# Optimization experiments

Measured on AMD Instinct MI355X. Metric: run time of the kernel, lower is better.

The kernel has to match this reference:

```python
import jax, jax.numpy as jnp
import numpy as np

N = 20000      # nodes
E = 640000     # edges (avg degree 32)
IN = 32        # input_dim
HID = 256      # hidden_dim
H = 8          # num_heads
Dh = HID // H  # head_dim = 32
TD = 32        # time_dim
L = 3          # num_layers
OUT = 2


def setup_inputs() -> dict:
    key = jax.random.key(0)
    ks = jax.random.split(key, 20)
    def w(k, sh):
        return (jax.random.normal(k, sh, jnp.float32) * 0.05)
    return {
        "x": jax.random.normal(ks[0], (N, IN), jnp.float32),
        "timestamps": jax.random.uniform(ks[1], (N,), jnp.float32),
        "edge_index": jax.random.randint(ks[2], (2, E), 0, N, jnp.int32),
        "batch": jnp.zeros((N,), jnp.int32),
        "time_freq": jax.random.normal(ks[3], (TD // 2,), jnp.float32),
        "inW": w(ks[4], (IN, HID)), "inb": jnp.zeros((HID,), jnp.float32),
        "qW": w(ks[5], (L, HID + TD, HID)), "qb": jnp.zeros((L, HID), jnp.float32),
        "kW": w(ks[6], (L, HID + TD, HID)), "kb": jnp.zeros((L, HID), jnp.float32),
        "vW": w(ks[7], (L, HID, HID)), "vb": jnp.zeros((L, HID), jnp.float32),
        "oW": w(ks[8], (L, HID, HID)), "ob": jnp.zeros((L, HID), jnp.float32),
        "c1W": w(ks[9], (HID, HID // 2)), "c1b": jnp.zeros((HID // 2,), jnp.float32),
        "c2W": w(ks[10], (HID // 2, OUT)), "c2b": jnp.zeros((OUT,), jnp.float32),
    }


def reference(x, timestamps, time_freq, inW, inb, qW, qb, kW, kb, vW, vb,
              oW, ob, c1W, c1b, c2W, c2b, edge_index, batch):
    n = x.shape[0]
    src, dst = edge_index[0], edge_index[1]

    # Functional time encoding (node-level timestamps branch)
    t = (timestamps - timestamps.min()) / (timestamps.max() - timestamps.min() + 1e-8)
    wt = t[:, None] * time_freq[None, :]                      # [N, TD/2]
    tf = jnp.concatenate([jnp.cos(wt), jnp.sin(wt)], axis=-1)  # [N, TD]

    h = x @ inW + inb                                          # [N, HID]
    scale = 1.0 / np.sqrt(Dh).astype(np.float32)

    for l in range(L):
        xt = jnp.concatenate([h, tf], axis=-1)                 # [N, HID+TD]
        Q = (xt @ qW[l] + qb[l]).reshape(n, H, Dh)
        K = (xt @ kW[l] + kb[l]).reshape(n, H, Dh)
        V = (h @ vW[l] + vb[l]).reshape(n, H, Dh)

        # per-edge attention scores [E, H]
        scores = jnp.einsum('ehd,ehd->eh', Q[dst], K[src]) * scale

        # segment softmax over incoming edges of each dst node
        m = jax.ops.segment_max(scores, dst, num_segments=n)   # [N, H]
        e = jnp.exp(scores - m[dst])
        s = jax.ops.segment_sum(e, dst, num_segments=n)        # [N, H]
        att = e / s[dst]                                       # [E, H]

        msgs = att[..., None] * V[src]                         # [E, H, Dh]
        out = jax.ops.segment_sum(msgs, dst, num_segments=n)   # [N, H, Dh]
        out = out.reshape(n, HID) @ oW[l] + ob[l]
        h = jax.nn.elu(out)

    # global mean pool (single graph: batch all zeros)
    cnt = jax.ops.segment_sum(jnp.ones((n, 1), h.dtype), batch, num_segments=1)
    g = jax.ops.segment_sum(h, batch, num_segments=1) / jnp.maximum(cnt, 1.0)

    logits = jax.nn.relu(g @ c1W + c1b) @ c2W + c2b            # [1, OUT]
    return logits
```

## Files before the change

### kernel.cpp

```cpp
#include <hip/hip_runtime.h>
#include <math.h>

#define HID 256
#define TD 32
#define NL 3
#define C1DIM 128
#define OUTDIM 2
#define QKVW 768

using half8  = __attribute__((ext_vector_type(8))) _Float16;
using half2v = __attribute__((ext_vector_type(2))) _Float16;
using f32x4  = __attribute__((ext_vector_type(4))) float;

typedef __attribute__((address_space(1))) void gbl_void_t;
typedef __attribute__((address_space(3))) void lds_void_t;

__device__ __forceinline__ void load16_to_lds(const void* g, void* l) {
  __builtin_amdgcn_global_load_lds((const gbl_void_t*)g, (lds_void_t*)l, 16, 0, 0);
}

__device__ __forceinline__ float dot8h(half8 a, half8 b, float acc) {
#if __has_builtin(__builtin_amdgcn_fdot2)
  union { half8 v; half2v h2[4]; } ua, ub;
  ua.v = a; ub.v = b;
#pragma unroll
  for (int j = 0; j < 4; ++j) acc = __builtin_amdgcn_fdot2(ua.h2[j], ub.h2[j], acc, false);
  return acc;
#else
#pragma unroll
  for (int j = 0; j < 8; ++j) acc += (float)a[j] * (float)b[j];
  return acc;
#endif
}

__global__ __launch_bounds__(1024) void k_tsmm(const float* __restrict__ ts,
                                               float* __restrict__ mmf,
                                               int* __restrict__ deg, int n) {
  int t = threadIdx.x;
  float lmin = INFINITY, lmax = -INFINITY;
  for (int i = t; i < n; i += 1024) {
    float v = ts[i];
    lmin = fminf(lmin, v);
    lmax = fmaxf(lmax, v);
    deg[i] = 0;
  }
#pragma unroll
  for (int off = 32; off >= 1; off >>= 1) {
    lmin = fminf(lmin, __shfl_xor(lmin, off));
    lmax = fmaxf(lmax, __shfl_xor(lmax, off));
  }
  __shared__ float wmin[16], wmax[16];
  int lane = t & 63, w = t >> 6;
  if (lane == 0) { wmin[w] = lmin; wmax[w] = lmax; }
  __syncthreads();
  if (t == 0) {
    float a = INFINITY, b = -INFINITY;
    for (int i = 0; i < 16; ++i) { a = fminf(a, wmin[i]); b = fmaxf(b, wmax[i]); }
    mmf[0] = a; mmf[1] = b;
  }
}

__global__ void k_enc(const float* __restrict__ ts, const float* __restrict__ freq,
                      const float* __restrict__ mmf, const float* __restrict__ x,
                      _Float16* __restrict__ tfh, _Float16* __restrict__ xh, int n) {
  int idx = blockIdx.x * blockDim.x + threadIdx.x;
  int nt = n * TD;
  if (idx < nt) {
    int node = idx >> 5, j = idx & 31;
    float t = (ts[node] - mmf[0]) / (mmf[1] - mmf[0] + 1e-8f);
    float w = t * freq[j & 15];
    tfh[idx] = (_Float16)((j < 16) ? cosf(w) : sinf(w));
  } else if (idx < nt + n * 32) {
    int i2 = idx - nt;
    xh[i2] = (_Float16)x[i2];
  }
}

#define NB_QKV (NL * 9 * 12)
#define NB_O   (NL * 8 * 4)
#define NB_B   9

__global__ __launch_bounds__(256) void k_prep2(
    const float* __restrict__ qW, const float* __restrict__ kW,
    const float* __restrict__ vW, const float* __restrict__ oW,
    const float* __restrict__ qb, const float* __restrict__ kb,
    const float* __restrict__ vb,
    _Float16* __restrict__ qkvWt, float* __restrict__ qkvb,
    _Float16* __restrict__ oWt) {
  __shared__ _Float16 lds[32][65];
  int bid = blockIdx.x;
  int t = threadIdx.x;
  const int KQ = HID + TD;

  if (bid < NB_QKV) {
    int l = bid / 108;
    int rem = bid - l * 108;
    int kt = rem / 12, ntile = rem - kt * 12;
    int k0 = kt * 32, n0 = ntile * 64;
#pragma unroll
    for (int it = 0; it < 8; ++it) {
      int i = it * 256 + t;
      int kk = i >> 6, nn = i & 63;
      int k = k0 + kk, nrow = n0 + nn;
      float v;
      if (nrow < 256)      v = qW[(size_t)l * KQ * HID + (size_t)k * HID + nrow];
      else if (nrow < 512) v = kW[(size_t)l * KQ * HID + (size_t)k * HID + (nrow - 256)];
      else                 v = (k < HID) ? vW[(size_t)l * HID * HID + (size_t)k * HID + (nrow - 512)] : 0.f;
      lds[kk][nn] = (_Float16)v;
    }
    __syncthreads();
    {
      int nn = t >> 2, kq = (t & 3) * 8;
      _Float16* dst = qkvWt + (size_t)l * QKVW * KQ + (size_t)(n0 + nn) * KQ + k0 + kq;
      half8 v;
#pragma unroll
      for (int j = 0; j < 8; ++j) v[j] = lds[kq + j][nn];
      *(half8*)dst = v;
    }
    return;
  }
  bid -= NB_QKV;

  if (bid < NB_O) {
    int l = bid / 32;
    int rem = bid - l * 32;
    int kt = rem / 4, ntile = rem - kt * 4;
    int k0 = kt * 32, n0 = ntile * 64;
#pragma unroll
    for (int it = 0; it < 8; ++it) {
      int i = it * 256 + t;
      int kk = i >> 6, nn = i & 63;
      lds[kk][nn] = (_Float16)oW[(size_t)l * HID * HID + (size_t)(k0 + kk) * HID + n0 + nn];
    }
    __syncthreads();
    {
      int nn = t >> 2, kq = (t & 3) * 8;
      _Float16* dst = oWt + (size_t)l * HID * HID + (size_t)(n0 + nn) * HID + k0 + kq;
      half8 v;
#pragma unroll
      for (int j = 0; j < 8; ++j) v[j] = lds[kq + j][nn];
      *(half8*)dst = v;
    }
    return;
  }
  bid -= NB_O;

  {
    int idx = bid * 256 + t;
    if (idx < NL * QKVW) {
      int l = idx / QKVW;
      int j = idx - l * QKVW;
      float v;
      if (j < 256)      v = qb[l * HID + j];
      else if (j < 512) v = kb[l * HID + (j - 256)];
      else              v = vb[l * HID + (j - 512)];
      qkvb[idx] = v;
    }
  }
}

__global__ __launch_bounds__(256) void k_fold(const float* __restrict__ inW,
                                              const float* __restrict__ inb,
                                              const float* __restrict__ qW,
                                              const float* __restrict__ kW,
                                              const float* __restrict__ vW,
                                              const float* __restrict__ qb,
                                              const float* __restrict__ kb,
                                              const float* __restrict__ vb,
                                              _Float16* __restrict__ WcT,
                                              float* __restrict__ bc) {
  int idx = blockIdx.x * 256 + threadIdx.x;
  if (idx >= 65 * QKVW) return;
  int j = idx / QKVW;
  int nrow = idx - j * QKVW;
  auto W0 = [&](int c, int nr) -> float {
    if (nr < 256)      return qW[(size_t)c * HID + nr];
    else if (nr < 512) return kW[(size_t)c * HID + (nr - 256)];
    else               return vW[(size_t)c * HID + (nr - 512)];
  };
  if (j < 32) {
    float acc = 0.f;
    for (int c = 0; c < 256; ++c) acc += inW[j * HID + c] * W0(c, nrow);
    WcT[(size_t)nrow * 64 + j] = (_Float16)acc;
  } else if (j < 64) {
    int r = 256 + (j - 32);
    float v = 0.f;
    if (nrow < 256)      v = qW[(size_t)r * HID + nrow];
    else if (nrow < 512) v = kW[(size_t)r * HID + (nrow - 256)];
    WcT[(size_t)nrow * 64 + j] = (_Float16)v;
  } else {
    float acc;
    if (nrow < 256)      acc = qb[nrow];
    else if (nrow < 512) acc = kb[nrow - 256];
    else                 acc = vb[nrow - 512];
    for (int c = 0; c < 256; ++c) acc += inb[c] * W0(c, nrow);
    bc[nrow] = acc;
  }
}

__global__ void k_count(const int* __restrict__ dst, int* deg, int e) {
  int i = blockIdx.x * blockDim.x + threadIdx.x;
  if (i < e) atomicAdd(&deg[dst[i]], 1);
}

__global__ __launch_bounds__(256) void k_scan_part(const int* __restrict__ deg,
                                                   int* __restrict__ bsum, int n) {
  int t = threadIdx.x;
  int idx = blockIdx.x * 256 + t;
  int v = (idx < n) ? deg[idx] : 0;
  int lane = t & 63, w = t >> 6;
  int x = v;
#pragma unroll
  for (int off = 1; off < 64; off <<= 1) {
    int y = __shfl_up(x, off);
    if (lane >= off) x += y;
  }
  __shared__ int ws[4];
  if (lane == 63) ws[w] = x;
  __syncthreads();
  if (t == 0) bsum[blockIdx.x] = ws[0] + ws[1] + ws[2] + ws[3];
}

__global__ __launch_bounds__(64) void k_scan_mid(const int* __restrict__ bsum,
                                                 int* __restrict__ boff, int nb) {
  int lane = threadIdx.x;
  int carry = 0;
  for (int base = 0; base < nb; base += 64) {
    int i = base + lane;
    int v = (i < nb) ? bsum[i] : 0;
    int x = v;
#pragma unroll
    for (int off = 1; off < 64; off <<= 1) {
      int y = __shfl_up(x, off);
      if (lane >= off) x += y;
    }
    if (i < nb) boff[i] = carry + x - v;
    carry += __shfl(x, 63);
  }
}

__global__ __launch_bounds__(256) void k_scan_apply(const int* __restrict__ deg,
                                                    const int* __restrict__ boff,
                                                    int* __restrict__ row_ptr,
                                                    int* __restrict__ cursor, int n, int e) {
  int t = threadIdx.x;
  int idx = blockIdx.x * 256 + t;
  int v = (idx < n) ? deg[idx] : 0;
  int lane = t & 63, w = t >> 6;
  int x = v;
#pragma unroll
  for (int off = 1; off < 64; off <<= 1) {
    int y = __shfl_up(x, off);
    if (lane >= off) x += y;
  }
  __shared__ int ws[4];
  if (lane == 63) ws[w] = x;
  __syncthreads();
  int wpre = 0;
  for (int i = 0; i < w; ++i) wpre += ws[i];
  if (idx < n) {
    row_ptr[idx] = boff[blockIdx.x] + wpre + x - v;
    cursor[idx] = 0;
  }
  if (idx == 0) row_ptr[n] = e;
}

__global__ void k_scatter(const int* __restrict__ src, const int* __restrict__ dst,
                          const int* __restrict__ row_ptr, int* cursor,
                          int* __restrict__ colbuf, int e) {
  int i = blockIdx.x * blockDim.x + threadIdx.x;
  if (i >= e) return;
  int d = dst[i];
  int p = atomicAdd(&cursor[d], 1);
  colbuf[row_ptr[d] + p] = src[i];
}

__global__ __launch_bounds__(256) void k_gemm_f16(
    const _Float16* __restrict__ A1, int K1,
    const _Float16* __restrict__ A2, int K2,
    const _Float16* __restrict__ Bt,
    const float* __restrict__ bias,
    _Float16* __restrict__ C,
    int M, int Ncols, int Ktot, int mode) {
  __shared__ half8 smem8[2 * 768];
  char* smem = (char*)smem8;
  const int tid = threadIdx.x;
  const int lane = tid & 63, wave = tid >> 6;
  const int wm = wave >> 1, wn = wave & 1;
  const int row0 = blockIdx.y * 128;
  const int col0 = blockIdx.x * 64;

  auto stage = [&](int buf, int k0) {
    char* sA = smem + buf * 12288;
    char* sB = sA + 8192;
#pragma unroll
    for (int i = 0; i < 2; ++i) {
      int kg = i * 2 + (wave >> 1);
      int row = (wave & 1) * 64 + lane;
      int grow = row0 + row; if (grow > M - 1) grow = M - 1;
      int k = k0 + kg * 8;
      const _Float16* src = (k < K1) ? (A1 + (size_t)grow * K1 + k)
                                     : (A2 + (size_t)grow * K2 + (k - K1));
      load16_to_lds(src, sA + (i * 256 + wave * 64) * 16);
    }
    {
      const _Float16* src = Bt + (size_t)(col0 + lane) * Ktot + k0 + wave * 8;
      load16_to_lds(src, sB + wave * 64 * 16);
    }
  };

  f32x4 acc[4][2];
#pragma unroll
  for (int mf = 0; mf < 4; ++mf)
#pragma unroll
    for (int nf = 0; nf < 2; ++nf) acc[mf][nf] = f32x4{0.f, 0.f, 0.f, 0.f};

  const int nsteps = Ktot >> 5;
  int cur = 0;
  stage(0, 0);
  __syncthreads();
  for (int st = 0; st < nsteps; ++st) {
    if (st + 1 < nsteps) stage(cur ^ 1, (st + 1) * 32);
    char* sA = smem + cur * 12288;
    char* sB = sA + 8192;
    half8 af[4], bf[2];
#pragma unroll
    for (int mf = 0; mf < 4; ++mf) {
      int slot = (lane >> 4) * 128 + wm * 64 + mf * 16 + (lane & 15);
      af[mf] = *(const half8*)(sA + slot * 16);
    }
#pragma unroll
    for (int nf = 0; nf < 2; ++nf) {
      int slot = (lane >> 4) * 64 + wn * 32 + nf * 16 + (lane & 15);
      bf[nf] = *(const half8*)(sB + slot * 16);
    }
#pragma unroll
    for (int mf = 0; mf < 4; ++mf)
#pragma unroll
      for (int nf = 0; nf < 2; ++nf)
        acc[mf][nf] = __builtin_amdgcn_mfma_f32_16x16x32_f16(af[mf], bf[nf], acc[mf][nf], 0, 0, 0);
    __syncthreads();
    cur ^= 1;
  }

  const int rbase = row0 + wm * 64 + (lane >> 4) * 4;
  const int cbase = col0 + wn * 32 + (lane & 15);
#pragma unroll
  for (int nf = 0; nf < 2; ++nf) {
    int col = cbase + nf * 16;
    float bv = bias[col];
#pragma unroll
    for (int mf = 0; mf < 4; ++mf) {
#pragma unroll
      for (int r = 0; r < 4; ++r) {
        int row = rbase + mf * 16 + r;
        if (row < M) {
          float v = acc[mf][nf][r] + bv;
          if (mode == 1) v = (v > 0.f) ? v : expm1f(v);
          C[(size_t)row * Ncols + col] = (_Float16)v;
        }
      }
    }
  }
}

__global__ __launch_bounds__(256) void k_gemm_qkv32(
    const _Float16* __restrict__ A1, int K1,
    const _Float16* __restrict__ A2, int K2,
    const _Float16* __restrict__ Bt,
    const float* __restrict__ bias,
    _Float16* __restrict__ Qb,
    _Float16* __restrict__ KV,
    int M, int Ktot, int R) {
  __shared__ half8 smem8[2 * 640];
  char* smem = (char*)smem8;
  int b = blockIdx.x;
  int xcd = b & 7;
  int idx = b >> 3;
  int rowt, colt;
  if (idx < 2 * R) { rowt = idx >> 1; colt = 8 + xcd + 8 * (idx & 1); }
  else             { rowt = idx - 2 * R; colt = xcd; }
  const int row0 = rowt * 128;
  const int col0 = colt * 32;
  const int tid = threadIdx.x;
  const int lane = tid & 63, wave = tid >> 6;

  auto stage = [&](int buf, int k0) {
    char* sA = smem + buf * 10240;
    char* sB = sA + 8192;
#pragma unroll
    for (int i = 0; i < 2; ++i) {
      int kg = i * 2 + (wave >> 1);
      int row = (wave & 1) * 64 + lane;
      int grow = row0 + row; if (grow > M - 1) grow = M - 1;
      int k = k0 + kg * 8;
      const _Float16* src = (k < K1) ? (A1 + (size_t)grow * K1 + k)
                                     : (A2 + (size_t)grow * K2 + (k - K1));
      load16_to_lds(src, sA + (i * 256 + wave * 64) * 16);
    }
    if (lane < 32) {
      const _Float16* src = Bt + (size_t)(col0 + lane) * Ktot + k0 + wave * 8;
      load16_to_lds(src, sB + (wave * 32 + lane) * 16);
    }
  };

  f32x4 acc[2][2];
#pragma unroll
  for (int mf = 0; mf < 2; ++mf)
#pragma unroll
    for (int nf = 0; nf < 2; ++nf) acc[mf][nf] = f32x4{0.f, 0.f, 0.f, 0.f};

  const int nsteps = Ktot >> 5;
  int cur = 0;
  stage(0, 0);
  __syncthreads();
  for (int st = 0; st < nsteps; ++st) {
    if (st + 1 < nsteps) stage(cur ^ 1, (st + 1) * 32);
    char* sA = smem + cur * 10240;
    char* sB = sA + 8192;
    half8 af[2], bf[2];
#pragma unroll
    for (int mf = 0; mf < 2; ++mf) {
      int slot = (lane >> 4) * 128 + wave * 32 + mf * 16 + (lane & 15);
      af[mf] = *(const half8*)(sA + slot * 16);
    }
#pragma unroll
    for (int nf = 0; nf < 2; ++nf) {
      int slot = (lane >> 4) * 32 + nf * 16 + (lane & 15);
      bf[nf] = *(const half8*)(sB + slot * 16);
    }
#pragma unroll
    for (int mf = 0; mf < 2; ++mf)
#pragma unroll
      for (int nf = 0; nf < 2; ++nf)
        acc[mf][nf] = __builtin_amdgcn_mfma_f32_16x16x32_f16(af[mf], bf[nf], acc[mf][nf], 0, 0, 0);
    __syncthreads();
    cur ^= 1;
  }

  const int rbase = row0 + wave * 32 + (lane >> 4) * 4;
  const int lcol = lane & 15;
#pragma unroll
  for (int nf = 0; nf < 2; ++nf) {
    int cg = col0 + nf * 16 + lcol;
    float bv = bias[cg];
    int dim = nf * 16 + lcol + (col0 & 31);
#pragma unroll
    for (int mf = 0; mf < 2; ++mf) {
#pragma unroll
      for (int r = 0; r < 4; ++r) {
        int row = rbase + mf * 16 + r;
        if (row < M) {
          float v = acc[mf][nf][r] + bv;
          if (colt < 8) {
            Qb[(size_t)row * HID + cg] = (_Float16)v;
          } else {
            int isV = colt >= 16;
            int hh = colt - (isV ? 16 : 8);
            KV[((size_t)hh * M + row) * 64 + isV * 32 + dim] = (_Float16)v;
          }
        }
      }
    }
  }
}

__global__ __launch_bounds__(256) void k_attn(const _Float16* __restrict__ Qb,
                                              const _Float16* __restrict__ KV,
                                              const int* __restrict__ row_ptr,
                                              const int* __restrict__ colbuf,
                                              _Float16* __restrict__ out, int n) {
  int h = blockIdx.x & 7;
  int node = (blockIdx.x >> 3) * 64 + (threadIdx.x >> 2);
  if (node >= n) return;
  int j = threadIdx.x & 3;
  const float scale = 0.17677669529663687f;
  const _Float16* KVh = KV + ((size_t)h * n) * 64;

  half8 qh = *(const half8*)(Qb + (size_t)node * HID + h * 32 + j * 8);
  half8 qs;
#pragma unroll
  for (int q = 0; q < 8; ++q) qs[q] = (_Float16)((float)qh[q] * scale);

  int beg = row_ptr[node], end = row_ptr[node + 1];
  float m = -INFINITY, s = 0.f;
  float a[8] = {0.f, 0.f, 0.f, 0.f, 0.f, 0.f, 0.f, 0.f};

  for (int i = beg; i < end; i += 4) {
    half8 kk[4], vv[4];
#pragma unroll
    for (int t = 0; t < 4; ++t) {
      int ii = i + t; if (ii > end - 1) ii = end - 1;
      int sn = colbuf[ii];
      const _Float16* b = KVh + ((size_t)sn) * 64 + j * 8;
      kk[t] = *(const half8*)(b);
      vv[t] = *(const half8*)(b + 32);
    }
    float p[4];
#pragma unroll
    for (int t = 0; t < 4; ++t) p[t] = dot8h(qs, kk[t], 0.f);
#pragma unroll
    for (int t = 0; t < 4; ++t) {
      p[t] += __shfl_xor(p[t], 1);
      p[t] += __shfl_xor(p[t], 2);
      if (i + t >= end) p[t] = -INFINITY;
    }
#pragma unroll
    for (int t = 0; t < 4; ++t) {
      float sc_ = p[t];
      if (sc_ <= m) {
        float e2 = __expf(sc_ - m);
        s += e2;
#pragma unroll
        for (int q = 0; q < 8; ++q) a[q] = fmaf(e2, (float)vv[t][q], a[q]);
      } else {
        float f = __expf(m - sc_);
        s = s * f + 1.f;
#pragma unroll
        for (int q = 0; q < 8; ++q) a[q] = fmaf(a[q], f, (float)vv[t][q]);
        m = sc_;
      }
    }
  }

  float inv = (s > 0.f) ? (1.f / s) : 0.f;
  half8 o;
#pragma unroll
  for (int q = 0; q < 8; ++q) o[q] = (_Float16)(a[q] * inv);
  *(half8*)(out + (size_t)node * HID + h * 32 + j * 8) = o;
}

__global__ __launch_bounds__(256) void k_pool_partial(const _Float16* __restrict__ h,
                                                      float* __restrict__ partial, int n) {
  int b = blockIdx.x, t = threadIdx.x;
  float s = 0.f;
  for (int r = b; r < n; r += 256) s += (float)h[(size_t)r * HID + t];
  partial[b * HID + t] = s;
}

__global__ __launch_bounds__(256) void k_final(const float* __restrict__ partial,
                                               const float* __restrict__ c1W,
                                               const float* __restrict__ c1b,
                                               const float* __restrict__ c2W,
                                               const float* __restrict__ c2b,
                                               float* __restrict__ out, int n) {
  __shared__ float gl[HID];
  __shared__ float r1[C1DIM];
  int t = threadIdx.x;
  float s = 0.f;
  for (int b = 0; b < 256; b++) s += partial[b * HID + t];
  gl[t] = s / (float)n;
  __syncthreads();
  if (t < C1DIM) {
    float a = c1b[t];
    for (int k = 0; k < HID; k++) a += gl[k] * c1W[k * C1DIM + t];
    r1[t] = fmaxf(a, 0.f);
  }
  __syncthreads();
  if (t < OUTDIM) {
    float a = c2b[t];
    for (int k = 0; k < C1DIM; k++) a += r1[k] * c2W[k * OUTDIM + t];
    out[t] = a;
  }
}

extern "C" void kernel_launch(void* const* d_in, const int* in_sizes, int n_in,
                              void* d_out, int out_size, void* d_ws, size_t ws_size,
                              hipStream_t stream) {
  const float* x    = (const float*)d_in[0];
  const float* ts   = (const float*)d_in[1];
  const int*   ei   = (const int*)d_in[2];
  const float* freq = (const float*)d_in[4];
  const float* inW  = (const float*)d_in[5];
  const float* inb  = (const float*)d_in[6];
  const float* qW   = (const float*)d_in[7];
  const float* qb   = (const float*)d_in[8];
  const float* kW   = (const float*)d_in[9];
  const float* kb   = (const float*)d_in[10];
  const float* vW   = (const float*)d_in[11];
  const float* vb   = (const float*)d_in[12];
  const float* oW   = (const float*)d_in[13];
  const float* ob   = (const float*)d_in[14];
  const float* c1W  = (const float*)d_in[15];
  const float* c1b  = (const float*)d_in[16];
  const float* c2W  = (const float*)d_in[17];
  const float* c2b  = (const float*)d_in[18];

  int n = in_sizes[1];
  int e = in_sizes[2] / 2;
  const int* src = ei;
  const int* dst = ei + e;
  int nb = (n + 255) / 256;
  int R = (n + 127) / 128;

  char* w = (char*)d_ws;
  size_t off = 0;
  auto alloc = [&](size_t bytes) -> char* {
    char* p = w + off;
    off = (off + bytes + 255) & ~(size_t)255;
    return p;
  };
  _Float16* tfh     = (_Float16*)alloc((size_t)n * TD * 2);
  _Float16* xh      = (_Float16*)alloc((size_t)n * 32 * 2);
  _Float16* h       = (_Float16*)alloc((size_t)n * HID * 2);
  _Float16* Qbuf    = (_Float16*)alloc((size_t)n * HID * 2);
  _Float16* KV      = (_Float16*)alloc((size_t)n * 512 * 2);
  _Float16* ao      = (_Float16*)alloc((size_t)n * HID * 2);
  _Float16* qkvWt   = (_Float16*)alloc((size_t)NL * QKVW * (HID + TD) * 2);
  float*    qkvb    = (float*)alloc((size_t)NL * QKVW * 4);
  _Float16* oWt     = (_Float16*)alloc((size_t)NL * HID * HID * 2);
  _Float16* WcT     = (_Float16*)alloc((size_t)QKVW * 64 * 2);
  float*    bc      = (float*)alloc((size_t)QKVW * 4);
  int*      deg     = (int*)alloc((size_t)n * 4);
  int*      cursor  = (int*)alloc((size_t)n * 4);
  int*      row_ptr = (int*)alloc((size_t)(n + 1) * 4);
  int*      colbuf  = (int*)alloc((size_t)e * 4);
  int*      bsum    = (int*)alloc((size_t)nb * 4);
  int*      boff    = (int*)alloc((size_t)nb * 4);
  float*    partial = (float*)alloc((size_t)256 * HID * 4);
  float*    mmf     = (float*)alloc(256);

  int b256 = 256;
  hipLaunchKernelGGL(k_tsmm, dim3(1), dim3(1024), 0, stream, ts, mmf, deg, n);
  hipLaunchKernelGGL(k_enc, dim3((n * 64 + 255) / 256), dim3(b256), 0, stream,
                     ts, freq, mmf, x, tfh, xh, n);
  hipLaunchKernelGGL(k_prep2, dim3(NB_QKV + NB_O + NB_B), dim3(b256), 0, stream,
                     qW, kW, vW, oW, qb, kb, vb, qkvWt, qkvb, oWt);
  hipLaunchKernelGGL(k_fold, dim3((65 * QKVW + 255) / 256), dim3(b256), 0, stream,
                     inW, inb, qW, kW, vW, qb, kb, vb, WcT, bc);
  hipLaunchKernelGGL(k_count, dim3((e + 255) / 256), dim3(b256), 0, stream, dst, deg, e);
  hipLaunchKernelGGL(k_scan_part, dim3(nb), dim3(b256), 0, stream, deg, bsum, n);
  hipLaunchKernelGGL(k_scan_mid, dim3(1), dim3(64), 0, stream, bsum, boff, nb);
  hipLaunchKernelGGL(k_scan_apply, dim3(nb), dim3(b256), 0, stream, deg, boff, row_ptr, cursor, n, e);
  hipLaunchKernelGGL(k_scatter, dim3((e + 255) / 256), dim3(b256), 0, stream, src, dst, row_ptr, cursor, colbuf, e);

  dim3 ggrid_h(HID / 64, (n + 127) / 128);
  int nchunks = (n + 63) / 64;
  for (int l = 0; l < NL; ++l) {
    const float*    qkvbl = qkvb + (size_t)l * QKVW;
    const _Float16* oWtl  = oWt + (size_t)l * HID * HID;
    if (l == 0) {
      hipLaunchKernelGGL(k_gemm_qkv32, dim3(24 * R), dim3(b256), 0, stream,
                         xh, 32, tfh, 32, WcT, bc, Qbuf, KV, n, 64, R);
    } else {
      const _Float16* qkvWtl = qkvWt + (size_t)l * QKVW * (HID + TD);
      hipLaunchKernelGGL(k_gemm_qkv32, dim3(24 * R), dim3(b256), 0, stream,
                         h, HID, tfh, TD, qkvWtl, qkvbl, Qbuf, KV, n, HID + TD, R);
    }
    hipLaunchKernelGGL(k_attn, dim3(nchunks * 8), dim3(b256), 0, stream,
                       Qbuf, KV, row_ptr, colbuf, ao, n);
    hipLaunchKernelGGL(k_gemm_f16, ggrid_h, dim3(b256), 0, stream,
                       ao, HID, ao, HID, oWtl, ob + l * HID, h, n, HID, HID, 1);
  }

  hipLaunchKernelGGL(k_pool_partial, dim3(256), dim3(b256), 0, stream, h, partial, n);
  hipLaunchKernelGGL(k_final, dim3(1), dim3(b256), 0, stream, partial, c1W, c1b, c2W, c2b, (float*)d_out, n);
}
```

Baseline: 490.7 us.

## Widen QKV GEMM tiles to 128x64 with permuted interleaved K/V weight columns

The fused QKV projection GEMM now uses 128x64 output tiles, with each of the four waves computing a 64x32 sub-tile, instead of 128x32 tiles. To support this, the QKV weight and bias columns are permuted during preprocessing so that each 64-column tile past the Q block holds one head's K and V together. This halves the number of blocks and increases reuse of each staged A tile. The trade-off is more registers and LDS per block, fewer blocks in flight, and a more involved XCD-aware block mapping with early-exit blocks.

```diff
diff --git a/kernel.cpp b/kernel.cpp
--- a/kernel.cpp
+++ b/kernel.cpp
@@ -31,6 +31,12 @@
   for (int j = 0; j < 8; ++j) acc += (float)a[j] * (float)b[j];
   return acc;
 #endif
+}
+
+__device__ __forceinline__ int ipermc(int c) {
+  if (c < 256) return c;
+  int t = c - 256, h = t >> 6, w = t & 63, isV = w >> 5, d = w & 31;
+  return 256 + isV * 256 + h * 32 + d;
 }
 
 __global__ __launch_bounds__(1024) void k_tsmm(const float* __restrict__ ts,
@@ -101,11 +107,12 @@
     for (int it = 0; it < 8; ++it) {
       int i = it * 256 + t;
       int kk = i >> 6, nn = i & 63;
-      int k = k0 + kk, nrow = n0 + nn;
+      int k = k0 + kk;
+      int orig = ipermc(n0 + nn);
       float v;
-      if (nrow < 256)      v = qW[(size_t)l * KQ * HID + (size_t)k * HID + nrow];
-      else if (nrow < 512) v = kW[(size_t)l * KQ * HID + (size_t)k * HID + (nrow - 256)];
-      else                 v = (k < HID) ? vW[(size_t)l * HID * HID + (size_t)k * HID + (nrow - 512)] : 0.f;
+      if (orig < 256)      v = qW[(size_t)l * KQ * HID + (size_t)k * HID + orig];
+      else if (orig < 512) v = kW[(size_t)l * KQ * HID + (size_t)k * HID + (orig - 256)];
+      else                 v = (k < HID) ? vW[(size_t)l * HID * HID + (size_t)k * HID + (orig - 512)] : 0.f;
       lds[kk][nn] = (_Float16)v;
     }
     __syncthreads();
@@ -150,10 +157,11 @@
     if (idx < NL * QKVW) {
       int l = idx / QKVW;
       int j = idx - l * QKVW;
+      int orig = ipermc(j);
       float v;
-      if (j < 256)      v = qb[l * HID + j];
-      else if (j < 512) v = kb[l * HID + (j - 256)];
-      else              v = vb[l * HID + (j - 512)];
+      if (orig < 256)      v = qb[l * HID + orig];
+      else if (orig < 512) v = kb[l * HID + (orig - 256)];
+      else                 v = vb[l * HID + (orig - 512)];
       qkvb[idx] = v;
     }
   }
@@ -172,7 +180,8 @@
   int idx = blockIdx.x * 256 + threadIdx.x;
   if (idx >= 65 * QKVW) return;
   int j = idx / QKVW;
-  int nrow = idx - j * QKVW;
+  int nrowP = idx - j * QKVW;
+  int orig = ipermc(nrowP);
   auto W0 = [&](int c, int nr) -> float {
     if (nr < 256)      return qW[(size_t)c * HID + nr];
     else if (nr < 512) return kW[(size_t)c * HID + (nr - 256)];
@@ -180,21 +189,21 @@
   };
   if (j < 32) {
     float acc = 0.f;
-    for (int c = 0; c < 256; ++c) acc += inW[j * HID + c] * W0(c, nrow);
-    WcT[(size_t)nrow * 64 + j] = (_Float16)acc;
+    for (int c = 0; c < 256; ++c) acc += inW[j * HID + c] * W0(c, orig);
+    WcT[(size_t)nrowP * 64 + j] = (_Float16)acc;
   } else if (j < 64) {
     int r = 256 + (j - 32);
     float v = 0.f;
-    if (nrow < 256)      v = qW[(size_t)r * HID + nrow];
-    else if (nrow < 512) v = kW[(size_t)r * HID + (nrow - 256)];
-    WcT[(size_t)nrow * 64 + j] = (_Float16)v;
+    if (orig < 256)      v = qW[(size_t)r * HID + orig];
+    else if (orig < 512) v = kW[(size_t)r * HID + (orig - 256)];
+    WcT[(size_t)nrowP * 64 + j] = (_Float16)v;
   } else {
     float acc;
-    if (nrow < 256)      acc = qb[nrow];
-    else if (nrow < 512) acc = kb[nrow - 256];
-    else                 acc = vb[nrow - 512];
-    for (int c = 0; c < 256; ++c) acc += inb[c] * W0(c, nrow);
-    bc[nrow] = acc;
+    if (orig < 256)      acc = qb[orig];
+    else if (orig < 512) acc = kb[orig - 256];
+    else                 acc = vb[orig - 512];
+    for (int c = 0; c < 256; ++c) acc += inb[c] * W0(c, orig);
+    bc[nrowP] = acc;
   }
 }
 
@@ -364,7 +373,7 @@
   }
 }
 
-__global__ __launch_bounds__(256) void k_gemm_qkv32(
+__global__ __launch_bounds__(256) void k_gemm_qkvp(
     const _Float16* __restrict__ A1, int K1,
     const _Float16* __restrict__ A2, int K2,
     const _Float16* __restrict__ Bt,
@@ -372,41 +381,45 @@
     _Float16* __restrict__ Qb,
     _Float16* __restrict__ KV,
     int M, int Ktot, int R) {
-  __shared__ half8 smem8[2 * 640];
+  int xcd = blockIdx.x & 7;
+  int i = blockIdx.x >> 3;
+  int ct, rowt;
+  if (i < R) { ct = 4 + xcd; rowt = i; }
+  else {
+    int j = (i - R) * 8 + xcd;
+    if (j >= 4 * R) return;
+    ct = j & 3; rowt = j >> 2;
+  }
+  __shared__ half8 smem8[2 * 768];
   char* smem = (char*)smem8;
-  int b = blockIdx.x;
-  int xcd = b & 7;
-  int idx = b >> 3;
-  int rowt, colt;
-  if (idx < 2 * R) { rowt = idx >> 1; colt = 8 + xcd + 8 * (idx & 1); }
-  else             { rowt = idx - 2 * R; colt = xcd; }
-  const int row0 = rowt * 128;
-  const int col0 = colt * 32;
   const int tid = threadIdx.x;
   const int lane = tid & 63, wave = tid >> 6;
+  const int wm = wave >> 1, wn = wave & 1;
+  const int row0 = rowt * 128;
+  const int col0 = ct * 64;
 
   auto stage = [&](int buf, int k0) {
-    char* sA = smem + buf * 10240;
+    char* sA = smem + buf * 12288;
     char* sB = sA + 8192;
 #pragma unroll
-    for (int i = 0; i < 2; ++i) {
-      int kg = i * 2 + (wave >> 1);
+    for (int ii = 0; ii < 2; ++ii) {
+      int kg = ii * 2 + (wave >> 1);
       int row = (wave & 1) * 64 + lane;
       int grow = row0 + row; if (grow > M - 1) grow = M - 1;
       int k = k0 + kg * 8;
       const _Float16* src = (k < K1) ? (A1 + (size_t)grow * K1 + k)
                                      : (A2 + (size_t)grow * K2 + (k - K1));
-      load16_to_lds(src, sA + (i * 256 + wave * 64) * 16);
-    }
-    if (lane < 32) {
+      load16_to_lds(src, sA + (ii * 256 + wave * 64) * 16);
+    }
+    {
       const _Float16* src = Bt + (size_t)(col0 + lane) * Ktot + k0 + wave * 8;
-      load16_to_lds(src, sB + (wave * 32 + lane) * 16);
+      load16_to_lds(src, sB + wave * 64 * 16);
     }
   };
 
-  f32x4 acc[2][2];
-#pragma unroll
-  for (int mf = 0; mf < 2; ++mf)
+  f32x4 acc[4][2];
+#pragma unroll
+  for (int mf = 0; mf < 4; ++mf)
 #pragma unroll
     for (int nf = 0; nf < 2; ++nf) acc[mf][nf] = f32x4{0.f, 0.f, 0.f, 0.f};
 
@@ -416,21 +429,21 @@
   __syncthreads();
   for (int st = 0; st < nsteps; ++st) {
     if (st + 1 < nsteps) stage(cur ^ 1, (st + 1) * 32);
-    char* sA = smem + cur * 10240;
+    char* sA = smem + cur * 12288;
     char* sB = sA + 8192;
-    half8 af[2], bf[2];
-#pragma unroll
-    for (int mf = 0; mf < 2; ++mf) {
-      int slot = (lane >> 4) * 128 + wave * 32 + mf * 16 + (lane & 15);
+    half8 af[4], bf[2];
+#pragma unroll
+    for (int mf = 0; mf < 4; ++mf) {
+      int slot = (lane >> 4) * 128 + wm * 64 + mf * 16 + (lane & 15);
       af[mf] = *(const half8*)(sA + slot * 16);
     }
 #pragma unroll
     for (int nf = 0; nf < 2; ++nf) {
-      int slot = (lane >> 4) * 32 + nf * 16 + (lane & 15);
+      int slot = (lane >> 4) * 64 + wn * 32 + nf * 16 + (lane & 15);
       bf[nf] = *(const half8*)(sB + slot * 16);
     }
 #pragma unroll
-    for (int mf = 0; mf < 2; ++mf)
+    for (int mf = 0; mf < 4; ++mf)
 #pragma unroll
       for (int nf = 0; nf < 2; ++nf)
         acc[mf][nf] = __builtin_amdgcn_mfma_f32_16x16x32_f16(af[mf], bf[nf], acc[mf][nf], 0, 0, 0);
@@ -438,27 +451,24 @@
     cur ^= 1;
   }
 
-  const int rbase = row0 + wave * 32 + (lane >> 4) * 4;
-  const int lcol = lane & 15;
+  const int rbase = row0 + wm * 64 + (lane >> 4) * 4;
+  const int cbase = col0 + wn * 32 + (lane & 15);
 #pragma unroll
   for (int nf = 0; nf < 2; ++nf) {
-    int cg = col0 + nf * 16 + lcol;
-    float bv = bias[cg];
-    int dim = nf * 16 + lcol + (col0 & 31);
-#pragma unroll
-    for (int mf = 0; mf < 2; ++mf) {
+    int col = cbase + nf * 16;
+    float bv = bias[col];
+    int w = col - col0;
+    int isV = w >> 5, d = w & 31;
+    int hh = ct - 4;
+#pragma unroll
+    for (int mf = 0; mf < 4; ++mf) {
 #pragma unroll
       for (int r = 0; r < 4; ++r) {
         int row = rbase + mf * 16 + r;
         if (row < M) {
           float v = acc[mf][nf][r] + bv;
-          if (colt < 8) {
-            Qb[(size_t)row * HID + cg] = (_Float16)v;
-          } else {
-            int isV = colt >= 16;
-            int hh = colt - (isV ? 16 : 8);
-            KV[((size_t)hh * M + row) * 64 + isV * 32 + dim] = (_Float16)v;
-          }
+          if (ct < 4) Qb[(size_t)row * HID + col] = (_Float16)v;
+          else        KV[((size_t)hh * M + row) * 64 + isV * 32 + d] = (_Float16)v;
         }
       }
     }
@@ -592,6 +602,7 @@
   const int* dst = ei + e;
   int nb = (n + 255) / 256;
   int R = (n + 127) / 128;
+  int qkv_grid = 8 * (R + (R + 1) / 2);
 
   char* w = (char*)d_ws;
   size_t off = 0;
@@ -640,11 +651,11 @@
     const float*    qkvbl = qkvb + (size_t)l * QKVW;
     const _Float16* oWtl  = oWt + (size_t)l * HID * HID;
     if (l == 0) {
-      hipLaunchKernelGGL(k_gemm_qkv32, dim3(24 * R), dim3(b256), 0, stream,
+      hipLaunchKernelGGL(k_gemm_qkvp, dim3(qkv_grid), dim3(b256), 0, stream,
                          xh, 32, tfh, 32, WcT, bc, Qbuf, KV, n, 64, R);
     } else {
       const _Float16* qkvWtl = qkvWt + (size_t)l * QKVW * (HID + TD);
-      hipLaunchKernelGGL(k_gemm_qkv32, dim3(24 * R), dim3(b256), 0, stream,
+      hipLaunchKernelGGL(k_gemm_qkvp, dim3(qkv_grid), dim3(b256), 0, stream,
                          h, HID, tfh, TD, qkvWtl, qkvbl, Qbuf, KV, n, HID + TD, R);
     }
     hipLaunchKernelGGL(k_attn, dim3(nchunks * 8), dim3(b256), 0, stream,
```

Result: no change. 482.0 us (-1.8%).
